# Kernel optimization log

Measured on AMD Instinct MI355X. Metric: run time of the kernel, lower is better.

The kernel has to match this reference:

```python
import jax, jax.numpy as jnp
import numpy as np

NUM_NODES = 50000
NUM_HYPEREDGES = 10000
NUM_INCIDENCES = 800000
CHANNELS = 256
NEG_SLOPE = 0.01  # torch leaky_relu default negative_slope


def setup_inputs() -> dict:
    key = jax.random.key(0)
    k_n, k_e, k_emb, k_cw, k_lw, k_lb = jax.random.split(key, 6)
    node_idx = jax.random.randint(k_n, (NUM_INCIDENCES,), 0, NUM_NODES, dtype=jnp.int32)
    edge_idx = jax.random.randint(k_e, (NUM_INCIDENCES,), 0, NUM_HYPEREDGES, dtype=jnp.int32)
    edge_index = jnp.stack([node_idx, edge_idx], axis=0)  # [2, nnz] incidence list
    s = 1.0 / np.sqrt(CHANNELS).astype(np.float32)
    emb = jax.random.normal(k_emb, (NUM_NODES, CHANNELS), jnp.float32)  # Node2Vec embedding table
    conv_w = jax.random.normal(k_cw, (CHANNELS, CHANNELS), jnp.float32) * s  # HypergraphConv.lin (no bias)
    conv_b = jnp.zeros((CHANNELS,), jnp.float32)  # HypergraphConv.bias
    lin_w = jax.random.normal(k_lw, (CHANNELS, CHANNELS), jnp.float32) * s
    lin_b = jax.random.normal(k_lb, (CHANNELS,), jnp.float32) * s
    return {"emb": emb, "conv_w": conv_w, "conv_b": conv_b,
            "lin_w": lin_w, "lin_b": lin_b, "edge_index": edge_index}


def reference(emb, conv_w, conv_b, lin_w, lin_b, edge_index):
    node_idx, edge_idx = edge_index[0], edge_index[1]
    # HypergraphConv (use_attention=False): X' = D^-1 H B^-1 H^T (X W^T) + b
    x = emb @ conv_w.T  # [N, C]
    ones = jnp.ones((NUM_INCIDENCES,), x.dtype)
    D = jax.ops.segment_sum(ones, node_idx, num_segments=NUM_NODES)       # node degree
    Dinv = jnp.where(D > 0, 1.0 / D, 0.0)
    B = jax.ops.segment_sum(ones, edge_idx, num_segments=NUM_HYPEREDGES)  # hyperedge degree
    Binv = jnp.where(B > 0, 1.0 / B, 0.0)
    # node -> hyperedge aggregation
    e = jax.ops.segment_sum(x[node_idx], edge_idx, num_segments=NUM_HYPEREDGES) * Binv[:, None]  # [E, C]
    # hyperedge -> node aggregation
    n = jax.ops.segment_sum(e[edge_idx], node_idx, num_segments=NUM_NODES) * Dinv[:, None] + conv_b  # [N, C]
    y = jax.nn.leaky_relu(n, NEG_SLOPE)
    g = y.T @ y  # [C, C] Gram
    out = jax.nn.leaky_relu(g @ lin_w.T + lin_b, NEG_SLOPE)
    return out
```

## Files before the change

kernel.cpp:

```cpp
#include <hip/hip_runtime.h>

#define N_NODES 50000
#define N_EDGES 10000
#define NNZ     800000
#define C       256
#define SLOPE   0.01f
#define KTOT    50176
#define KCHUNK  512
#define NZB     98
#define MPAD    10048

#define NB      250
#define EB_E    40
#define EB_N    200
#define CHUNK   3125
#define CAP     6000
#define MP_E    288
#define MP_N    1408

#define EAGG_G  628
#define NAGG_G  784

#define OFF_CC_E    0
#define OFF_CC_N    1024
#define OFF_CUR_E   2048
#define OFF_CUR_N   3072
#define OFF_DEG_E   4096
#define OFF_DEG_N   45056
#define ZERO_BYTES  245760
#define OFF_CB_E    266240
#define OFF_CB_N    267264
#define OFF_RS_N    268288
#define OFF_RS_E    468480
#define OFF_BUF_E   508672
#define OFF_BUF_N   3708672
#define OFF_CSR_E   6908672
#define OFF_CSR_N   10108672
#define OFF_EMBH    13308672
#define OFF_YT      13308672
#define OFF_EACC    39000064
#define OFF_E2      44144640
#define OFF_CWH     49289216
#define OFF_PART    49420288

typedef __attribute__((ext_vector_type(8))) short short8;
typedef __attribute__((ext_vector_type(4))) float floatx4;

static __device__ __forceinline__ unsigned short f2bf(float f) {
    unsigned int u = __float_as_uint(f);
    u = (u + 0x7fffu + ((u >> 16) & 1u)) >> 16;
    return (unsigned short)u;
}

static __device__ __forceinline__ void acc_bf8(const uint4 d, float* a) {
    a[0] += __uint_as_float(d.x << 16);
    a[1] += __uint_as_float(d.x & 0xffff0000u);
    a[2] += __uint_as_float(d.y << 16);
    a[3] += __uint_as_float(d.y & 0xffff0000u);
    a[4] += __uint_as_float(d.z << 16);
    a[5] += __uint_as_float(d.z & 0xffff0000u);
    a[6] += __uint_as_float(d.w << 16);
    a[7] += __uint_as_float(d.w & 0xffff0000u);
}

static __device__ __forceinline__ void idx8(const uint4 pk, int* ix) {
    ix[0] = (int)(pk.x & 0xffffu); ix[1] = (int)(pk.x >> 16);
    ix[2] = (int)(pk.y & 0xffffu); ix[3] = (int)(pk.y >> 16);
    ix[4] = (int)(pk.z & 0xffffu); ix[5] = (int)(pk.z >> 16);
    ix[6] = (int)(pk.w & 0xffffu); ix[7] = (int)(pk.w >> 16);
}

__global__ __launch_bounds__(256) void zero_kernel(float4* __restrict__ p, int n4) {
    int i = blockIdx.x * 256 + threadIdx.x;
    if (i < n4) p[i] = make_float4(0.f, 0.f, 0.f, 0.f);
}

#define PREP_EMB_BLOCKS 6251
#define PREP_CW_BLOCKS  32
__global__ __launch_bounds__(256) void prep_kernel(const float4* __restrict__ emb4,
                                                   uint4* __restrict__ embh4,
                                                   const float4* __restrict__ cw4,
                                                   uint4* __restrict__ cwh4,
                                                   const int* __restrict__ node_idx,
                                                   const int* __restrict__ edge_idx,
                                                   int* __restrict__ cc_e,
                                                   int* __restrict__ cc_n) {
    __shared__ int he[NB], hn[NB];
    int b = blockIdx.x, tid = threadIdx.x;
    if (b < PREP_EMB_BLOCKS) {
        int i = b * 256 + tid;
        if (i >= 1600032) return;
        uint4 o = {0u, 0u, 0u, 0u};
        if (i < 1600000) {
            float4 f0 = emb4[2 * i], f1 = emb4[2 * i + 1];
            o.x = f2bf(f0.x) | ((unsigned)f2bf(f0.y) << 16);
            o.y = f2bf(f0.z) | ((unsigned)f2bf(f0.w) << 16);
            o.z = f2bf(f1.x) | ((unsigned)f2bf(f1.y) << 16);
            o.w = f2bf(f1.z) | ((unsigned)f2bf(f1.w) << 16);
        }
        int node = i >> 5, c = i & 31;
        embh4[(size_t)(((c >> 2) * 50001 + node) << 2) + (c & 3)] = o;
    } else if (b < PREP_EMB_BLOCKS + PREP_CW_BLOCKS) {
        int i = (b - PREP_EMB_BLOCKS) * 256 + tid;
        float4 f0 = cw4[2 * i], f1 = cw4[2 * i + 1];
        uint4 o;
        o.x = f2bf(f0.x) | ((unsigned)f2bf(f0.y) << 16);
        o.y = f2bf(f0.z) | ((unsigned)f2bf(f0.w) << 16);
        o.z = f2bf(f1.x) | ((unsigned)f2bf(f1.y) << 16);
        o.w = f2bf(f1.z) | ((unsigned)f2bf(f1.w) << 16);
        cwh4[i] = o;
    } else {
        int base = (b - PREP_EMB_BLOCKS - PREP_CW_BLOCKS) * CHUNK;
        for (int i = tid; i < NB; i += 256) { he[i] = 0; hn[i] = 0; }
        __syncthreads();
        for (int i = tid; i < CHUNK; i += 256) {
            atomicAdd(&he[edge_idx[base + i] / EB_E], 1);
            atomicAdd(&hn[node_idx[base + i] / EB_N], 1);
        }
        __syncthreads();
        for (int k = tid; k < NB; k += 256) {
            if (he[k]) atomicAdd(&cc_e[k], he[k]);
            if (hn[k]) atomicAdd(&cc_n[k], hn[k]);
        }
    }
}

__global__ __launch_bounds__(256) void coarse_scan_kernel(const int* __restrict__ cc_e,
                                                          const int* __restrict__ cc_n,
                                                          int* __restrict__ cb_e,
                                                          int* __restrict__ cb_n) {
    __shared__ int tmp[256];
    int tid = threadIdx.x;
    int v = (tid < NB) ? cc_e[tid] : 0;
    tmp[tid] = v;
    __syncthreads();
    for (int off = 1; off < 256; off <<= 1) {
        int t = (tid >= off) ? tmp[tid - off] : 0;
        __syncthreads();
        tmp[tid] += t;
        __syncthreads();
    }
    if (tid < NB) cb_e[tid + 1] = tmp[tid];
    if (tid == 0) cb_e[0] = 0;
    __syncthreads();
    v = (tid < NB) ? cc_n[tid] : 0;
    tmp[tid] = v;
    __syncthreads();
    for (int off = 1; off < 256; off <<= 1) {
        int t = (tid >= off) ? tmp[tid - off] : 0;
        __syncthreads();
        tmp[tid] += t;
        __syncthreads();
    }
    if (tid < NB) cb_n[tid + 1] = tmp[tid];
    if (tid == 0) cb_n[0] = 0;
}

__global__ __launch_bounds__(256) void bucket_scatter_kernel(const int* __restrict__ node_idx,
                                                             const int* __restrict__ edge_idx,
                                                             const int* __restrict__ cb_e,
                                                             const int* __restrict__ cb_n,
                                                             int* __restrict__ cur_e,
                                                             int* __restrict__ cur_n,
                                                             int* __restrict__ buf_e,
                                                             int* __restrict__ buf_n) {
    __shared__ int he[NB], hn[NB], be[NB], bn[NB];
    int tid = threadIdx.x;
    int base = blockIdx.x * CHUNK;
    for (int i = tid; i < NB; i += 256) { he[i] = 0; hn[i] = 0; }
    __syncthreads();
    int pe[13], pn[13];
    #pragma unroll
    for (int k = 0; k < 13; k++) {
        int i = tid + k * 256;
        if (i < CHUNK) {
            int e = edge_idx[base + i], v = node_idx[base + i];
            int ke = e / EB_E, kn = v / EB_N;
            pe[k] = (ke << 12) | atomicAdd(&he[ke], 1);
            pn[k] = (kn << 12) | atomicAdd(&hn[kn], 1);
        }
    }
    __syncthreads();
    for (int k = tid; k < NB; k += 256) {
        int c = he[k];
        be[k] = cb_e[k] + (c ? atomicAdd(&cur_e[k], c) : 0);
        int cn = hn[k];
        bn[k] = cb_n[k] + (cn ? atomicAdd(&cur_n[k], cn) : 0);
    }
    __syncthreads();
    #pragma unroll
    for (int k = 0; k < 13; k++) {
        int i = tid + k * 256;
        if (i < CHUNK) {
            int e = edge_idx[base + i], v = node_idx[base + i];
            int ke = pe[k] >> 12, oe = pe[k] & 4095;
            buf_e[be[ke] + oe] = (v << 6) | (e - ke * EB_E);
            int kn = pn[k] >> 12, on = pn[k] & 4095;
            buf_n[bn[kn] + on] = (e << 8) | (v - kn * EB_N);
        }
    }
}

__global__ __launch_bounds__(256) void bucket_sort_kernel(const int* __restrict__ buf_e,
                                                          const int* __restrict__ buf_n,
                                                          const int* __restrict__ cb_e,
                                                          const int* __restrict__ cb_n,
                                                          unsigned short* __restrict__ csr_e,
                                                          unsigned short* __restrict__ csr_n,
                                                          int* __restrict__ rs_e,
                                                          int* __restrict__ rs_n,
                                                          int* __restrict__ deg_e,
                                                          int* __restrict__ deg_n) {
    __shared__ int A[CAP];
    __shared__ int h[EB_N], bs[EB_N], cs[EB_N];
    int tid = threadIdx.x;
    bool edgeSide = blockIdx.x < NB;
    int k = edgeSide ? blockIdx.x : blockIdx.x - NB;
    int eb = edgeSide ? EB_E : EB_N;
    int shift = edgeSide ? 6 : 8;
    int mask = (1 << shift) - 1;
    int mp = edgeSide ? MP_E : MP_N;
    int sent = edgeSide ? N_NODES : N_EDGES;
    const int* cb  = edgeSide ? cb_e : cb_n;
    const int* buf = edgeSide ? buf_e : buf_n;
    unsigned short* csr = edgeSide ? csr_e : csr_n;
    int* rs  = edgeSide ? rs_e : rs_n;
    int* deg = edgeSide ? deg_e : deg_n;
    int base = cb[k];
    int base_pad = (base + k * mp + 7) & ~7;
    int cnt = cb[k + 1] - base;
    for (int i = tid; i < eb; i += 256) h[i] = 0;
    __syncthreads();
    for (int i = tid; i < cnt; i += 256) {
        int it = buf[base + i];
        if (i < CAP) A[i] = it;
        atomicAdd(&h[it & mask], 1);
    }
    __syncthreads();
    if (tid == 0) {
        int s = 0;
        for (int j = 0; j < eb; j++) { bs[j] = s; s += (h[j] + 7) & ~7; }
    }
    __syncthreads();
    for (int j = tid; j < eb; j += 256) {
        rs[k * eb + j] = base_pad + bs[j];
        deg[k * eb + j] = h[j];
        cs[j] = h[j];
        h[j] = 0;
    }
    if (tid == 0 && k == NB - 1) rs[edgeSide ? N_EDGES : N_NODES] = NNZ;
    __syncthreads();
    for (int j = tid; j < eb; j += 256) {
        int c0 = cs[j], e0 = (c0 + 7) & ~7;
        for (int x = c0; x < e0; x++) csr[base_pad + bs[j] + x] = (unsigned short)sent;
    }
    for (int i = tid; i < cnt; i += 256) {
        int it = (i < CAP) ? A[i] : buf[base + i];
        int loc = it & mask;
        int off = bs[loc] + atomicAdd(&h[loc], 1);
        csr[base_pad + off] = (unsigned short)(it >> shift);
    }
}

__global__ __launch_bounds__(256) void edge_aggregate_kernel(const uint4* __restrict__ embh4,
                                                             const unsigned short* __restrict__ csr_e,
                                                             const int* __restrict__ rs_e,
                                                             const int* __restrict__ deg_e,
                                                             unsigned short* __restrict__ e_acc_h) {
    int sid = blockIdx.x & 7, g = blockIdx.x >> 3;
    const uint4* __restrict__ tbl = embh4 + (size_t)sid * 50001 * 4;
    const uint4* __restrict__ csr4 = (const uint4*)csr_e;
    int tid = threadIdx.x;
    int w = tid >> 6, lane = tid & 63;
    int grp = lane >> 4, q = (lane >> 2) & 3, c4 = lane & 3;
    int e = g * 16 + w * 4 + grp;
    int s = rs_e[e];
    int dg = deg_e[e];
    int c0 = s >> 3, nc = (dg + 7) >> 3;
    float a[8] = {0.f, 0.f, 0.f, 0.f, 0.f, 0.f, 0.f, 0.f};
    for (int c = c0 + q; c < c0 + nc; c += 4) {
        uint4 pk = csr4[c];
        int ix[8];
        idx8(pk, ix);
        #pragma unroll
        for (int j = 0; j < 8; j++) acc_bf8(tbl[ix[j] * 4 + c4], a);
    }
    #pragma unroll
    for (int off = 4; off <= 8; off <<= 1) {
        #pragma unroll
        for (int jj = 0; jj < 8; jj++) a[jj] += __shfl_xor(a[jj], off);
    }
    if (q == 0) {
        uint4 o;
        o.x = f2bf(a[0]) | ((unsigned)f2bf(a[1]) << 16);
        o.y = f2bf(a[2]) | ((unsigned)f2bf(a[3]) << 16);
        o.z = f2bf(a[4]) | ((unsigned)f2bf(a[5]) << 16);
        o.w = f2bf(a[6]) | ((unsigned)f2bf(a[7]) << 16);
        ((uint4*)(e_acc_h + (size_t)e * C + sid * 32))[c4] = o;
    }
}

__global__ __launch_bounds__(256) void edge_gemm_mfma_kernel(const unsigned short* __restrict__ e_acc_h,
                                                             const unsigned short* __restrict__ cwh,
                                                             const int* __restrict__ deg_e,
                                                             unsigned short* __restrict__ e2h) {
    __shared__ __align__(16) unsigned short As[64 * 72];
    __shared__ __align__(16) unsigned short Bs[64 * 72];
    int i0 = blockIdx.x * 64, j0 = blockIdx.y * 64;
    int tid = threadIdx.x;
    int w = tid >> 6, lane = tid & 63;
    int col = lane & 15, quad = lane >> 4;
    floatx4 acc[4] = {};
    for (int step = 0; step < 4; step++) {
        int kb = step * 64;
        __syncthreads();
        #pragma unroll
        for (int l = 0; l < 2; l++) {
            int slot = tid + l * 256;
            int row = slot >> 3, grp = slot & 7;
            uint4 da = *(const uint4*)(e_acc_h + (size_t)(i0 + row) * C + kb + grp * 8);
            *(uint4*)(&As[row * 72 + grp * 8]) = da;
            uint4 db = *(const uint4*)(cwh + (size_t)(j0 + row) * C + kb + grp * 8);
            *(uint4*)(&Bs[row * 72 + grp * 8]) = db;
        }
        __syncthreads();
        #pragma unroll
        for (int sub = 0; sub < 2; sub++) {
            short8 a = *(const short8*)(&As[(w * 16 + col) * 72 + sub * 32 + quad * 8]);
            #pragma unroll
            for (int jt = 0; jt < 4; jt++) {
                short8 b = *(const short8*)(&Bs[(jt * 16 + col) * 72 + sub * 32 + quad * 8]);
                acc[jt] = __builtin_amdgcn_mfma_f32_16x16x32_bf16(a, b, acc[jt], 0, 0, 0);
            }
        }
    }
    #pragma unroll
    for (int r = 0; r < 4; r++) {
        int m = i0 + w * 16 + quad * 4 + r;
        int dg = deg_e[m];
        float binv = (dg > 0) ? 1.0f / (float)dg : 0.0f;
        #pragma unroll
        for (int jt = 0; jt < 4; jt++) {
            int ch = j0 + jt * 16 + col;
            e2h[(size_t)((ch >> 5) * MPAD + m) * 32 + (ch & 31)] = f2bf(acc[jt][r] * binv);
        }
    }
}

__global__ __launch_bounds__(256) void node_aggregate_t_kernel(const uint4* __restrict__ e2h4,
                                                               const unsigned short* __restrict__ csr_n,
                                                               const int* __restrict__ rs_n,
                                                               const int* __restrict__ deg_n,
                                                               const float* __restrict__ conv_b,
                                                               unsigned short* __restrict__ yT) {
    __shared__ unsigned short T[32][66];
    int sid = blockIdx.x & 7, g = blockIdx.x >> 3;
    const uint4* __restrict__ tbl = e2h4 + (size_t)sid * MPAD * 4;
    const uint4* __restrict__ csr4 = (const uint4*)csr_n;
    int tid = threadIdx.x;
    int w = tid >> 6, lane = tid & 63;
    int q = lane >> 2, c4 = lane & 3;
    int n = g * 64 + w * 16 + q;
    int s = rs_n[min(n, N_NODES)];
    int dg = deg_n[n];
    int c0 = s >> 3, nc = (dg + 7) >> 3;
    float4 b0 = ((const float4*)conv_b)[sid * 8 + c4 * 2];
    float4 b1 = ((const float4*)conv_b)[sid * 8 + c4 * 2 + 1];
    float a[8] = {0.f, 0.f, 0.f, 0.f, 0.f, 0.f, 0.f, 0.f};
    for (int c = c0; c < c0 + nc; c++) {
        uint4 pk = csr4[c];
        int ix[8];
        idx8(pk, ix);
        #pragma unroll
        for (int j = 0; j < 8; j++) acc_bf8(tbl[ix[j] * 4 + c4], a);
    }
    float dinv = (dg > 0) ? 1.0f / (float)dg : 0.0f;
    float bb[8] = {b0.x, b0.y, b0.z, b0.w, b1.x, b1.y, b1.z, b1.w};
    #pragma unroll
    for (int jj = 0; jj < 8; jj++) {
        float r = a[jj] * dinv + bb[jj];
        r = (r > 0.f) ? r : SLOPE * r;
        if (n >= N_NODES) r = 0.f;
        T[c4 * 8 + jj][w * 16 + q] = f2bf(r);
    }
    __syncthreads();
    int rr = tid >> 3, cc = tid & 7;
    uint4 o;
    o.x = T[rr][cc * 8 + 0] | ((unsigned)T[rr][cc * 8 + 1] << 16);
    o.y = T[rr][cc * 8 + 2] | ((unsigned)T[rr][cc * 8 + 3] << 16);
    o.z = T[rr][cc * 8 + 4] | ((unsigned)T[rr][cc * 8 + 5] << 16);
    o.w = T[rr][cc * 8 + 6] | ((unsigned)T[rr][cc * 8 + 7] << 16);
    *(uint4*)(yT + (size_t)(sid * 32 + rr) * KTOT + g * 64 + cc * 8) = o;
}

__global__ __launch_bounds__(256) void gram_mfma_kernel(const unsigned short* __restrict__ yT,
                                                        float* __restrict__ part) {
    static const int PI[10] = {0, 0, 0, 0, 1, 1, 1, 2, 2, 3};
    static const int PJ[10] = {0, 1, 2, 3, 1, 2, 3, 2, 3, 3};
    __shared__ __align__(16) unsigned short As[64 * 72];
    __shared__ __align__(16) unsigned short Bs[64 * 72];
    int i0 = PI[blockIdx.x] * 64, j0 = PJ[blockIdx.x] * 64;
    bool diag = (i0 == j0);
    int kb0 = blockIdx.y * KCHUNK;
    int tid = threadIdx.x;
    int w = tid >> 6, lane = tid & 63;
    int col = lane & 15, quad = lane >> 4;
    floatx4 acc[4] = {};
    for (int step = 0; step < KCHUNK / 64; step++) {
        int kb = kb0 + step * 64;
        __syncthreads();
        #pragma unroll
        for (int l = 0; l < 2; l++) {
            int slot = tid + l * 256;
            int row = slot >> 3, grp = slot & 7;
            uint4 da = *(const uint4*)(yT + (size_t)(i0 + row) * KTOT + kb + grp * 8);
            *(uint4*)(&As[row * 72 + grp * 8]) = da;
            if (!diag) {
                uint4 db = *(const uint4*)(yT + (size_t)(j0 + row) * KTOT + kb + grp * 8);
                *(uint4*)(&Bs[row * 72 + grp * 8]) = db;
            }
        }
        __syncthreads();
        const unsigned short* Bb = diag ? As : Bs;
        #pragma unroll
        for (int sub = 0; sub < 2; sub++) {
            short8 a = *(const short8*)(&As[(w * 16 + col) * 72 + sub * 32 + quad * 8]);
            #pragma unroll
            for (int jt = 0; jt < 4; jt++) {
                short8 b = *(const short8*)(&Bb[(jt * 16 + col) * 72 + sub * 32 + quad * 8]);
                acc[jt] = __builtin_amdgcn_mfma_f32_16x16x32_bf16(a, b, acc[jt], 0, 0, 0);
            }
        }
    }
    float* slab = part + ((size_t)blockIdx.y * 10 + blockIdx.x) * 4096;
    #pragma unroll
    for (int jt = 0; jt < 4; jt++)
        #pragma unroll
        for (int r = 0; r < 4; r++)
            slab[(w * 16 + quad * 4 + r) * 64 + jt * 16 + col] = acc[jt][r];
}

__global__ __launch_bounds__(256) void greduce_out_kernel(const float* __restrict__ part,
                                                          const float* __restrict__ lin_w,
                                                          const float* __restrict__ lin_b,
                                                          float* __restrict__ out) {
    __shared__ float gs[C];
    int i = blockIdx.x, j = threadIdx.x;
    int a = i >> 6, b = j >> 6;
    int lo = min(a, b), hi = max(a, b);
    int t = lo * (7 - lo) / 2 + hi;
    int li = (a <= b) ? (i & 63) : (j & 63);
    int lj = (a <= b) ? (j & 63) : (i & 63);
    const float* p = part + (size_t)t * 4096 + li * 64 + lj;
    float s = 0.f;
    for (int z = 0; z < NZB; z++) s += p[(size_t)z * 40960];
    gs[j] = s;
    __syncthreads();
    float acc = lin_b[j];
    const float* wrow = lin_w + (size_t)j * C;
    for (int k = 0; k < C; k++) acc += gs[k] * wrow[k];
    out[(size_t)i * C + j] = (acc > 0.f) ? acc : SLOPE * acc;
}

extern "C" void kernel_launch(void* const* d_in, const int* in_sizes, int n_in,
                              void* d_out, int out_size, void* d_ws, size_t ws_size,
                              hipStream_t stream) {
    const float* emb    = (const float*)d_in[0];
    const float* conv_w = (const float*)d_in[1];
    const float* conv_b = (const float*)d_in[2];
    const float* lin_w  = (const float*)d_in[3];
    const float* lin_b  = (const float*)d_in[4];
    const int*   eidx   = (const int*)d_in[5];
    const int* node_idx = eidx;
    const int* edge_idx = eidx + NNZ;

    char* ws = (char*)d_ws;
    int* cc_e  = (int*)(ws + OFF_CC_E);
    int* cc_n  = (int*)(ws + OFF_CC_N);
    int* cur_e = (int*)(ws + OFF_CUR_E);
    int* cur_n = (int*)(ws + OFF_CUR_N);
    int* deg_e = (int*)(ws + OFF_DEG_E);
    int* deg_n = (int*)(ws + OFF_DEG_N);
    int* cb_e  = (int*)(ws + OFF_CB_E);
    int* cb_n  = (int*)(ws + OFF_CB_N);
    int* rs_n  = (int*)(ws + OFF_RS_N);
    int* rs_e  = (int*)(ws + OFF_RS_E);
    int* buf_e = (int*)(ws + OFF_BUF_E);
    int* buf_n = (int*)(ws + OFF_BUF_N);
    unsigned short* csr_e = (unsigned short*)(ws + OFF_CSR_E);
    unsigned short* csr_n = (unsigned short*)(ws + OFF_CSR_N);
    uint4* embh4 = (uint4*)(ws + OFF_EMBH);
    unsigned short* e_acc_h = (unsigned short*)(ws + OFF_EACC);
    unsigned short* e2h = (unsigned short*)(ws + OFF_E2);
    unsigned short* cwh = (unsigned short*)(ws + OFF_CWH);
    unsigned short* yT  = (unsigned short*)(ws + OFF_YT);
    float* part = (float*)(ws + OFF_PART);
    float* out = (float*)d_out;

    zero_kernel<<<ZERO_BYTES / 4096, 256, 0, stream>>>((float4*)ws, ZERO_BYTES / 16);

    prep_kernel<<<PREP_EMB_BLOCKS + PREP_CW_BLOCKS + 256, 256, 0, stream>>>(
        (const float4*)emb, embh4, (const float4*)conv_w, (uint4*)cwh,
        node_idx, edge_idx, cc_e, cc_n);

    coarse_scan_kernel<<<1, 256, 0, stream>>>(cc_e, cc_n, cb_e, cb_n);

    bucket_scatter_kernel<<<256, 256, 0, stream>>>(node_idx, edge_idx, cb_e, cb_n,
                                                   cur_e, cur_n, buf_e, buf_n);

    bucket_sort_kernel<<<2 * NB, 256, 0, stream>>>(buf_e, buf_n, cb_e, cb_n,
                                                   csr_e, csr_n, rs_e, rs_n,
                                                   deg_e, deg_n);

    edge_aggregate_kernel<<<8 * EAGG_G, 256, 0, stream>>>(embh4, csr_e, rs_e, deg_e, e_acc_h);

    edge_gemm_mfma_kernel<<<dim3(MPAD / 64, C / 64), 256, 0, stream>>>(e_acc_h, cwh, deg_e, e2h);

    node_aggregate_t_kernel<<<8 * NAGG_G, 256, 0, stream>>>((const uint4*)e2h, csr_n, rs_n,
                                                            deg_n, conv_b, yT);

    gram_mfma_kernel<<<dim3(10, NZB), 256, 0, stream>>>(yT, part);

    greduce_out_kernel<<<C, 256, 0, stream>>>(part, lin_w, lin_b, out);
}
```

Baseline: 267.7 us.

## Process two segments per thread in aggregation kernels with a grid-stride loop

The edge and node aggregation kernels now have each thread group gather two hyperedges or two nodes in interleaved loops. This doubles the independent gather loads in flight per thread, to better hide latency in these memory-bound gathers. The grids are shrunk and each block loops over several groups, and the bf16-to-float accumulation uses two-wide float vectors so the compiler can emit packed adds. The trade-offs are higher register pressure, load imbalance when the two paired segments differ in degree, and an extra barrier per loop iteration in the node kernel.

```diff
diff --git a/kernel.cpp b/kernel.cpp
--- a/kernel.cpp
+++ b/kernel.cpp
@@ -18,8 +18,8 @@
 #define MP_E    288
 #define MP_N    1408
 
-#define EAGG_G  628
-#define NAGG_G  784
+#define EAGG_B  157
+#define NAGG_B  196
 
 #define OFF_CC_E    0
 #define OFF_CC_N    1024
@@ -45,6 +45,7 @@
 
 typedef __attribute__((ext_vector_type(8))) short short8;
 typedef __attribute__((ext_vector_type(4))) float floatx4;
+typedef __attribute__((ext_vector_type(2))) float f32x2;
 
 static __device__ __forceinline__ unsigned short f2bf(float f) {
     unsigned int u = __float_as_uint(f);
@@ -52,15 +53,12 @@
     return (unsigned short)u;
 }
 
-static __device__ __forceinline__ void acc_bf8(const uint4 d, float* a) {
-    a[0] += __uint_as_float(d.x << 16);
-    a[1] += __uint_as_float(d.x & 0xffff0000u);
-    a[2] += __uint_as_float(d.y << 16);
-    a[3] += __uint_as_float(d.y & 0xffff0000u);
-    a[4] += __uint_as_float(d.z << 16);
-    a[5] += __uint_as_float(d.z & 0xffff0000u);
-    a[6] += __uint_as_float(d.w << 16);
-    a[7] += __uint_as_float(d.w & 0xffff0000u);
+static __device__ __forceinline__ void acc_bf8p(const uint4 d, f32x2* a) {
+    f32x2 v0 = { __uint_as_float(d.x << 16), __uint_as_float(d.x & 0xffff0000u) };
+    f32x2 v1 = { __uint_as_float(d.y << 16), __uint_as_float(d.y & 0xffff0000u) };
+    f32x2 v2 = { __uint_as_float(d.z << 16), __uint_as_float(d.z & 0xffff0000u) };
+    f32x2 v3 = { __uint_as_float(d.w << 16), __uint_as_float(d.w & 0xffff0000u) };
+    a[0] += v0; a[1] += v1; a[2] += v2; a[3] += v3;
 }
 
 static __device__ __forceinline__ void idx8(const uint4 pk, int* ix) {
@@ -267,36 +265,61 @@
                                                              const int* __restrict__ rs_e,
                                                              const int* __restrict__ deg_e,
                                                              unsigned short* __restrict__ e_acc_h) {
-    int sid = blockIdx.x & 7, g = blockIdx.x >> 3;
-    const uint4* __restrict__ tbl = embh4 + (size_t)sid * 50001 * 4;
+    int sid = blockIdx.x & 7, b = blockIdx.x >> 3;
     const uint4* __restrict__ csr4 = (const uint4*)csr_e;
     int tid = threadIdx.x;
     int w = tid >> 6, lane = tid & 63;
     int grp = lane >> 4, q = (lane >> 2) & 3, c4 = lane & 3;
-    int e = g * 16 + w * 4 + grp;
-    int s = rs_e[e];
-    int dg = deg_e[e];
-    int c0 = s >> 3, nc = (dg + 7) >> 3;
-    float a[8] = {0.f, 0.f, 0.f, 0.f, 0.f, 0.f, 0.f, 0.f};
-    for (int c = c0 + q; c < c0 + nc; c += 4) {
-        uint4 pk = csr4[c];
-        int ix[8];
-        idx8(pk, ix);
-        #pragma unroll
-        for (int j = 0; j < 8; j++) acc_bf8(tbl[ix[j] * 4 + c4], a);
-    }
-    #pragma unroll
-    for (int off = 4; off <= 8; off <<= 1) {
-        #pragma unroll
-        for (int jj = 0; jj < 8; jj++) a[jj] += __shfl_xor(a[jj], off);
-    }
-    if (q == 0) {
-        uint4 o;
-        o.x = f2bf(a[0]) | ((unsigned)f2bf(a[1]) << 16);
-        o.y = f2bf(a[2]) | ((unsigned)f2bf(a[3]) << 16);
-        o.z = f2bf(a[4]) | ((unsigned)f2bf(a[5]) << 16);
-        o.w = f2bf(a[6]) | ((unsigned)f2bf(a[7]) << 16);
-        ((uint4*)(e_acc_h + (size_t)e * C + sid * 32))[c4] = o;
+    const uint4* __restrict__ tbl = embh4 + (size_t)sid * 50001 * 4 + c4;
+    for (int gg = b; gg < 314; gg += EAGG_B) {
+        int e0 = gg * 32 + w * 8 + grp * 2;
+        int e1 = e0 + 1;
+        int s0 = rs_e[min(e0, N_EDGES)], d0 = deg_e[e0];
+        int s1 = rs_e[min(e1, N_EDGES)], d1 = deg_e[e1];
+        int c00 = s0 >> 3, nc0 = (d0 + 7) >> 3;
+        int c01 = s1 >> 3, nc1 = (d1 + 7) >> 3;
+        f32x2 aA[4] = {}, aB[4] = {};
+        int m = max(nc0, nc1);
+        for (int c = q; c < m; c += 4) {
+            if (c < nc0) {
+                uint4 pk = csr4[c00 + c];
+                int ix[8];
+                idx8(pk, ix);
+                #pragma unroll
+                for (int j = 0; j < 8; j++) acc_bf8p(tbl[(size_t)ix[j] * 4], aA);
+            }
+            if (c < nc1) {
+                uint4 pk = csr4[c01 + c];
+                int ix[8];
+                idx8(pk, ix);
+                #pragma unroll
+                for (int j = 0; j < 8; j++) acc_bf8p(tbl[(size_t)ix[j] * 4], aB);
+            }
+        }
+        #pragma unroll
+        for (int off = 4; off <= 8; off <<= 1) {
+            #pragma unroll
+            for (int j = 0; j < 4; j++) {
+                aA[j].x += __shfl_xor(aA[j].x, off); aA[j].y += __shfl_xor(aA[j].y, off);
+                aB[j].x += __shfl_xor(aB[j].x, off); aB[j].y += __shfl_xor(aB[j].y, off);
+            }
+        }
+        if (q == 0) {
+            uint4 o;
+            o.x = f2bf(aA[0].x) | ((unsigned)f2bf(aA[0].y) << 16);
+            o.y = f2bf(aA[1].x) | ((unsigned)f2bf(aA[1].y) << 16);
+            o.z = f2bf(aA[2].x) | ((unsigned)f2bf(aA[2].y) << 16);
+            o.w = f2bf(aA[3].x) | ((unsigned)f2bf(aA[3].y) << 16);
+            ((uint4*)(e_acc_h + (size_t)e0 * C + sid * 32))[c4] = o;
+        }
+        if (q == 1) {
+            uint4 o;
+            o.x = f2bf(aB[0].x) | ((unsigned)f2bf(aB[0].y) << 16);
+            o.y = f2bf(aB[1].x) | ((unsigned)f2bf(aB[1].y) << 16);
+            o.z = f2bf(aB[2].x) | ((unsigned)f2bf(aB[2].y) << 16);
+            o.w = f2bf(aB[3].x) | ((unsigned)f2bf(aB[3].y) << 16);
+            ((uint4*)(e_acc_h + (size_t)e1 * C + sid * 32))[c4] = o;
+        }
     }
 }
 
@@ -353,44 +376,76 @@
                                                                const int* __restrict__ deg_n,
                                                                const float* __restrict__ conv_b,
                                                                unsigned short* __restrict__ yT) {
-    __shared__ unsigned short T[32][66];
-    int sid = blockIdx.x & 7, g = blockIdx.x >> 3;
-    const uint4* __restrict__ tbl = e2h4 + (size_t)sid * MPAD * 4;
+    __shared__ unsigned short T[2][32][66];
+    int sid = blockIdx.x & 7, b = blockIdx.x >> 3;
     const uint4* __restrict__ csr4 = (const uint4*)csr_n;
     int tid = threadIdx.x;
     int w = tid >> 6, lane = tid & 63;
     int q = lane >> 2, c4 = lane & 3;
-    int n = g * 64 + w * 16 + q;
-    int s = rs_n[min(n, N_NODES)];
-    int dg = deg_n[n];
-    int c0 = s >> 3, nc = (dg + 7) >> 3;
+    const uint4* __restrict__ tbl = e2h4 + (size_t)sid * MPAD * 4 + c4;
     float4 b0 = ((const float4*)conv_b)[sid * 8 + c4 * 2];
     float4 b1 = ((const float4*)conv_b)[sid * 8 + c4 * 2 + 1];
-    float a[8] = {0.f, 0.f, 0.f, 0.f, 0.f, 0.f, 0.f, 0.f};
-    for (int c = c0; c < c0 + nc; c++) {
-        uint4 pk = csr4[c];
-        int ix[8];
-        idx8(pk, ix);
-        #pragma unroll
-        for (int j = 0; j < 8; j++) acc_bf8(tbl[ix[j] * 4 + c4], a);
-    }
-    float dinv = (dg > 0) ? 1.0f / (float)dg : 0.0f;
     float bb[8] = {b0.x, b0.y, b0.z, b0.w, b1.x, b1.y, b1.z, b1.w};
-    #pragma unroll
-    for (int jj = 0; jj < 8; jj++) {
-        float r = a[jj] * dinv + bb[jj];
-        r = (r > 0.f) ? r : SLOPE * r;
-        if (n >= N_NODES) r = 0.f;
-        T[c4 * 8 + jj][w * 16 + q] = f2bf(r);
-    }
-    __syncthreads();
-    int rr = tid >> 3, cc = tid & 7;
-    uint4 o;
-    o.x = T[rr][cc * 8 + 0] | ((unsigned)T[rr][cc * 8 + 1] << 16);
-    o.y = T[rr][cc * 8 + 2] | ((unsigned)T[rr][cc * 8 + 3] << 16);
-    o.z = T[rr][cc * 8 + 4] | ((unsigned)T[rr][cc * 8 + 5] << 16);
-    o.w = T[rr][cc * 8 + 6] | ((unsigned)T[rr][cc * 8 + 7] << 16);
-    *(uint4*)(yT + (size_t)(sid * 32 + rr) * KTOT + g * 64 + cc * 8) = o;
+    for (int p = b; p < 392; p += NAGG_B) {
+        int nA = p * 128 + w * 16 + q;
+        int nB = nA + 64;
+        int sA = rs_n[min(nA, N_NODES)], dA = deg_n[nA];
+        int sB = rs_n[min(nB, N_NODES)], dB = deg_n[nB];
+        int cA = sA >> 3, ncA = (dA + 7) >> 3;
+        int cB = sB >> 3, ncB = (dB + 7) >> 3;
+        f32x2 aA[4] = {}, aB[4] = {};
+        int m = max(ncA, ncB);
+        for (int c = 0; c < m; c++) {
+            if (c < ncA) {
+                uint4 pk = csr4[cA + c];
+                int ix[8];
+                idx8(pk, ix);
+                #pragma unroll
+                for (int j = 0; j < 8; j++) acc_bf8p(tbl[(size_t)ix[j] * 4], aA);
+            }
+            if (c < ncB) {
+                uint4 pk = csr4[cB + c];
+                int ix[8];
+                idx8(pk, ix);
+                #pragma unroll
+                for (int j = 0; j < 8; j++) acc_bf8p(tbl[(size_t)ix[j] * 4], aB);
+            }
+        }
+        float dinvA = (dA > 0) ? 1.0f / (float)dA : 0.0f;
+        float dinvB = (dB > 0) ? 1.0f / (float)dB : 0.0f;
+        #pragma unroll
+        for (int j = 0; j < 4; j++) {
+            float r0 = aA[j].x * dinvA + bb[2 * j];
+            float r1 = aA[j].y * dinvA + bb[2 * j + 1];
+            r0 = (r0 > 0.f) ? r0 : SLOPE * r0;
+            r1 = (r1 > 0.f) ? r1 : SLOPE * r1;
+            if (nA >= N_NODES) { r0 = 0.f; r1 = 0.f; }
+            T[0][c4 * 8 + 2 * j][w * 16 + q] = f2bf(r0);
+            T[0][c4 * 8 + 2 * j + 1][w * 16 + q] = f2bf(r1);
+            float r2 = aB[j].x * dinvB + bb[2 * j];
+            float r3 = aB[j].y * dinvB + bb[2 * j + 1];
+            r2 = (r2 > 0.f) ? r2 : SLOPE * r2;
+            r3 = (r3 > 0.f) ? r3 : SLOPE * r3;
+            if (nB >= N_NODES) { r2 = 0.f; r3 = 0.f; }
+            T[1][c4 * 8 + 2 * j][w * 16 + q] = f2bf(r2);
+            T[1][c4 * 8 + 2 * j + 1][w * 16 + q] = f2bf(r3);
+        }
+        __syncthreads();
+        int rr = tid >> 3, cc = tid & 7;
+        uint4 o;
+        o.x = T[0][rr][cc * 8 + 0] | ((unsigned)T[0][rr][cc * 8 + 1] << 16);
+        o.y = T[0][rr][cc * 8 + 2] | ((unsigned)T[0][rr][cc * 8 + 3] << 16);
+        o.z = T[0][rr][cc * 8 + 4] | ((unsigned)T[0][rr][cc * 8 + 5] << 16);
+        o.w = T[0][rr][cc * 8 + 6] | ((unsigned)T[0][rr][cc * 8 + 7] << 16);
+        *(uint4*)(yT + (size_t)(sid * 32 + rr) * KTOT + p * 128 + cc * 8) = o;
+        uint4 o2;
+        o2.x = T[1][rr][cc * 8 + 0] | ((unsigned)T[1][rr][cc * 8 + 1] << 16);
+        o2.y = T[1][rr][cc * 8 + 2] | ((unsigned)T[1][rr][cc * 8 + 3] << 16);
+        o2.z = T[1][rr][cc * 8 + 4] | ((unsigned)T[1][rr][cc * 8 + 5] << 16);
+        o2.w = T[1][rr][cc * 8 + 6] | ((unsigned)T[1][rr][cc * 8 + 7] << 16);
+        *(uint4*)(yT + (size_t)(sid * 32 + rr) * KTOT + p * 128 + 64 + cc * 8) = o2;
+        __syncthreads();
+    }
 }
 
 __global__ __launch_bounds__(256) void gram_mfma_kernel(const unsigned short* __restrict__ yT,
@@ -512,11 +567,11 @@
                                                    csr_e, csr_n, rs_e, rs_n,
                                                    deg_e, deg_n);
 
-    edge_aggregate_kernel<<<8 * EAGG_G, 256, 0, stream>>>(embh4, csr_e, rs_e, deg_e, e_acc_h);
+    edge_aggregate_kernel<<<8 * EAGG_B, 256, 0, stream>>>(embh4, csr_e, rs_e, deg_e, e_acc_h);
 
     edge_gemm_mfma_kernel<<<dim3(MPAD / 64, C / 64), 256, 0, stream>>>(e_acc_h, cwh, deg_e, e2h);
 
-    node_aggregate_t_kernel<<<8 * NAGG_G, 256, 0, stream>>>((const uint4*)e2h, csr_n, rs_n,
+    node_aggregate_t_kernel<<<8 * NAGG_B, 256, 0, stream>>>((const uint4*)e2h, csr_n, rs_n,
                                                             deg_n, conv_b, yT);
 
     gram_mfma_kernel<<<dim3(10, NZB), 256, 0, stream>>>(yT, part);
```

After: 275.2 us. 2.8% more time.
